# Performance work log

Measured on AMD Instinct MI355X. Metric: run time of the kernel, lower is better.

## Reference

```python
import jax, jax.numpy as jnp
import numpy as np

B, LV, LT, D, TD, H = 64, 1024, 128, 256, 1536, 4
HD = D // H
KEEP_RATIO = 0.5
K = min(max(int(np.ceil(LV * KEEP_RATIO)), 1), LV)
ND = LV - K  # number of dropped tokens
EPS_NORM = 1e-12


def setup_inputs() -> dict:
    key = jax.random.key(0)
    ks = jax.random.split(key, 9)
    s = 0.02
    return {
        "hidden_v": jax.random.normal(ks[0], (B, LV, D), jnp.float32),
        "hidden_t": jax.random.normal(ks[1], (B, LT, TD), jnp.float32),
        "senti_t": jax.random.normal(ks[2], (B, LT), jnp.float32),
        "mask_v": jnp.ones((B, LV), dtype=bool),
        "mask_t": jnp.ones((B, LT), dtype=bool),
        "W_t": jax.random.normal(ks[3], (D, TD), jnp.float32) * s,
        "b_t": jnp.zeros((D,), jnp.float32),
        "Wq": jax.random.normal(ks[4], (D, D), jnp.float32) * s,
        "bq": jnp.zeros((D,), jnp.float32),
        "Wk": jax.random.normal(ks[5], (D, D), jnp.float32) * s,
        "bk": jnp.zeros((D,), jnp.float32),
    }


def _l2norm(x):
    n = jnp.linalg.norm(x, axis=-1, keepdims=True)
    return x / jnp.maximum(n, EPS_NORM)


def _prune_one(V_b, score_b):
    """V_b: [LV, D], score_b: [LV] -> (V_merge [K, D], top_idx [K])."""
    _, top_idx = jax.lax.top_k(score_b, K)
    top_idx = jnp.sort(top_idx)
    V_keep = V_b[top_idx]                       # [K, D]
    drop_mask = jnp.ones((LV,), bool).at[top_idx].set(False)
    ar = jnp.arange(LV)
    drop_idx = jnp.sort(jnp.where(drop_mask, ar, LV + ar))[:ND]  # [ND], sorted
    V_drop = V_b[drop_idx]                      # [ND, D]
    score_drop = score_b[drop_idx]              # [ND]
    # bipartite cosine-similarity assignment of dropped -> kept
    sim = _l2norm(V_drop) @ _l2norm(V_keep).T   # [ND, K]
    assign = jnp.argmax(sim, axis=1)            # [ND]
    # per-cluster softmax over dropped-token scores (segment softmax)
    seg_max = jax.ops.segment_max(score_drop, assign, num_segments=K)
    w = jnp.exp(score_drop - seg_max[assign])
    denom = jax.ops.segment_sum(w, assign, num_segments=K)
    w = w / jnp.maximum(denom[assign], EPS_NORM)
    merged = jax.ops.segment_sum(w[:, None] * V_drop, assign, num_segments=K)
    has_member = jax.ops.segment_sum(jnp.ones((ND,), V_b.dtype), assign, num_segments=K) > 0
    V_merge = _l2norm(V_keep + merged)
    V_out = jnp.where(has_member[:, None], V_merge, V_keep)
    return V_out, top_idx


def reference(hidden_v, hidden_t, senti_t, mask_v, mask_t, W_t, b_t, Wq, bq, Wk, bk):
    mt = mask_t.astype(jnp.float32)
    # text projection + sentiment weights
    T = hidden_t @ W_t.T + b_t                                   # [B, LT, D]
    w_t = jnp.abs(senti_t) * mt
    w_t = w_t / (w_t.sum(axis=1, keepdims=True) + 1e-8)
    w_t = w_t * mt
    # cross-attention weights (averaged over heads); attn_out is unused by the module
    q = (hidden_v @ Wq.T + bq).reshape(B, LV, H, HD)
    k = (T @ Wk.T + bk).reshape(B, LT, H, HD)
    scores = jnp.einsum('bqhd,bkhd->bhqk', q, k) / np.sqrt(HD)   # [B, H, LV, LT]
    scores = jnp.where(mask_t[:, None, None, :], scores, -1e9)
    attn = jax.nn.softmax(scores, axis=-1).mean(axis=1)          # [B, LV, LT]
    score_v = jnp.einsum('bqk,bk->bq', attn, w_t)                # [B, LV]
    score_v = jnp.where(mask_v, score_v, -1e9)
    hidden_v_new, retained_indices = jax.vmap(_prune_one)(hidden_v, score_v)
    return hidden_v_new, retained_indices
```

## Files before the change

kernel.cpp:

```cpp
#include <hip/hip_runtime.h>
#include <math.h>

#define B_ 64
#define LV_ 1024
#define LT_ 128
#define D_ 256
#define TD_ 1536
#define H_ 4
#define HD_ 64
#define K_ 512
#define ND_ 512

__device__ float g_M[TD_ * D_];
__device__ float g_WqT[D_ * D_];
__device__ float g_WkT[D_ * D_];
__device__ float g_kbias[D_];
__device__ float g_wt[B_ * LT_];
__device__ float g_Kmat[(size_t)B_ * LT_ * D_];
__device__ float g_score[B_ * LV_];
__device__ int   g_tidx[B_ * K_];
__device__ int   g_didx[B_ * ND_];
__device__ float g_sdrop[B_ * ND_];
__device__ int   g_assign[B_ * ND_];
__device__ float g_kninv[B_ * K_];


__device__ __forceinline__ float f4c(const float4& v, int i) {
  return ((const float*)&v)[i];
}

__global__ __launch_bounds__(256) void prep1_kernel(
    const float* __restrict__ Wk, const float* __restrict__ Wq,
    const float* __restrict__ bt, const float* __restrict__ bk) {
  int bx = blockIdx.x, t = threadIdx.x;
  if (bx < D_) {
    g_WkT[bx * D_ + t] = Wk[t * D_ + bx];
  } else if (bx < 2 * D_) {
    int j = bx - D_;
    g_WqT[j * D_ + t] = Wq[t * D_ + j];
  } else {
    float acc = bk[t];
    for (int e = 0; e < D_; ++e) acc += bt[e] * Wk[t * D_ + e];
    g_kbias[t] = acc;
  }
}

__global__ __launch_bounds__(256) void prep2_kernel(const float* __restrict__ Wt) {
  int j0 = blockIdx.x * 16;
  int t = threadIdx.x;
  __shared__ float WtL[256 * 20];
  const float4* Wt4 = (const float4*)Wt;
#pragma unroll
  for (int i = 0; i < 4; ++i) {
    int idx = i * 256 + t;
    int e = idx >> 2, j4 = idx & 3;
    float4 v = Wt4[e * (TD_ / 4) + (j0 >> 2) + j4];
    WtL[e * 20 + 4 * j4 + 0] = v.x;
    WtL[e * 20 + 4 * j4 + 1] = v.y;
    WtL[e * 20 + 4 * j4 + 2] = v.z;
    WtL[e * 20 + 4 * j4 + 3] = v.w;
  }
  __syncthreads();
  float acc[16];
#pragma unroll
  for (int jj = 0; jj < 16; ++jj) acc[jj] = 0.f;
  for (int e = 0; e < D_; ++e) {
    float wk = g_WkT[e * D_ + t];
#pragma unroll
    for (int q4 = 0; q4 < 4; ++q4) {
      float4 w = *(const float4*)&WtL[e * 20 + 4 * q4];
      acc[4 * q4 + 0] += w.x * wk;
      acc[4 * q4 + 1] += w.y * wk;
      acc[4 * q4 + 2] += w.z * wk;
      acc[4 * q4 + 3] += w.w * wk;
    }
  }
#pragma unroll
  for (int jj = 0; jj < 16; ++jj) g_M[(j0 + jj) * D_ + t] = acc[jj];
}

__global__ __launch_bounds__(128) void wt_kernel(const float* __restrict__ senti) {
  int b = blockIdx.x, t = threadIdx.x;
  __shared__ float red[128];
  float v = fabsf(senti[b * LT_ + t]);
  red[t] = v;
  __syncthreads();
  for (int s = 64; s > 0; s >>= 1) {
    if (t < s) red[t] += red[t + s];
    __syncthreads();
  }
  g_wt[b * LT_ + t] = v / (red[0] + 1e-8f);
}

__global__ __launch_bounds__(256) void kproj_kernel(const float* __restrict__ ht) {
  int b = blockIdx.x >> 3;
  int l0 = (blockIdx.x & 7) * 16;
  int t = threadIdx.x;
  __shared__ float htT[256 * 20];
  int lq = t >> 6;
  int dq = t & 63;
  float acc[4][4];
#pragma unroll
  for (int li = 0; li < 4; ++li)
#pragma unroll
    for (int di = 0; di < 4; ++di) acc[li][di] = 0.f;
  const float4* M4 = (const float4*)g_M;
  const float4* ht4 = (const float4*)ht;
  for (int e0 = 0; e0 < TD_; e0 += 256) {
    __syncthreads();
#pragma unroll
    for (int i = 0; i < 4; ++i) {
      int idx = i * 256 + t;
      int e4 = idx >> 4, l = idx & 15;
      float4 v = ht4[(size_t)(b * LT_ + l0 + l) * (TD_ / 4) + (e0 >> 2) + e4];
      htT[(4 * e4 + 0) * 20 + l] = v.x;
      htT[(4 * e4 + 1) * 20 + l] = v.y;
      htT[(4 * e4 + 2) * 20 + l] = v.z;
      htT[(4 * e4 + 3) * 20 + l] = v.w;
    }
    __syncthreads();
    for (int e = 0; e < 256; ++e) {
      float4 m = M4[(size_t)(e0 + e) * 64 + dq];
      float4 hl = *(const float4*)&htT[e * 20 + 4 * lq];
#pragma unroll
      for (int li = 0; li < 4; ++li) {
        float hs = f4c(hl, li);
        acc[li][0] += hs * m.x;
        acc[li][1] += hs * m.y;
        acc[li][2] += hs * m.z;
        acc[li][3] += hs * m.w;
      }
    }
  }
  float4 kb = *(const float4*)(g_kbias + 4 * dq);
#pragma unroll
  for (int li = 0; li < 4; ++li) {
    float4 o = make_float4(acc[li][0] + kb.x, acc[li][1] + kb.y,
                           acc[li][2] + kb.z, acc[li][3] + kb.w);
    ((float4*)g_Kmat)[(size_t)(b * LT_ + l0 + 4 * lq + li) * 64 + dq] = o;
  }
}

__global__ __launch_bounds__(256, 3) void score_kernel(
    const float* __restrict__ hv, const float* __restrict__ bq) {
  int b = blockIdx.y;
  int q0 = blockIdx.x * 32;
  int t = threadIdx.x;
  __shared__ float qR[32 * 256];
  __shared__ float kT[32 * 128];
  int co = t & 31;
  int rq = t >> 5;
  {
    float acc[4][8];
#pragma unroll
    for (int c = 0; c < 8; ++c) {
      float bqv = bq[8 * co + c];
#pragma unroll
      for (int ri = 0; ri < 4; ++ri) acc[ri][c] = bqv;
    }
    const float4* hv4 = (const float4*)(hv + ((size_t)b * LV_ + q0) * D_);
    for (int j4 = 0; j4 < 64; ++j4) {
      float4 hq[4];
#pragma unroll
      for (int ri = 0; ri < 4; ++ri) hq[ri] = hv4[(4 * rq + ri) * 64 + j4];
#pragma unroll
      for (int jj = 0; jj < 4; ++jj) {
        const float4* w4 = (const float4*)(g_WqT + (4 * j4 + jj) * D_ + 8 * co);
        float4 wa = w4[0], wb = w4[1];
#pragma unroll
        for (int ri = 0; ri < 4; ++ri) {
          float hvv = f4c(hq[ri], jj);
          acc[ri][0] += hvv * wa.x;
          acc[ri][1] += hvv * wa.y;
          acc[ri][2] += hvv * wa.z;
          acc[ri][3] += hvv * wa.w;
          acc[ri][4] += hvv * wb.x;
          acc[ri][5] += hvv * wb.y;
          acc[ri][6] += hvv * wb.z;
          acc[ri][7] += hvv * wb.w;
        }
      }
    }
    float4* qR4w = (float4*)qR;
#pragma unroll
    for (int ri = 0; ri < 4; ++ri) {
      qR4w[(4 * rq + ri) * 64 + 2 * co + 0] =
          make_float4(acc[ri][0], acc[ri][1], acc[ri][2], acc[ri][3]);
      qR4w[(4 * rq + ri) * 64 + 2 * co + 1] =
          make_float4(acc[ri][4], acc[ri][5], acc[ri][6], acc[ri][7]);
    }
  }
  int qq = rq;
  int kq = co;
  float4 wtv = ((const float4*)(g_wt + b * LT_))[kq];
  float svacc[4] = {0.f, 0.f, 0.f, 0.f};
  const float4* km4 = ((const float4*)g_Kmat) + (size_t)b * LT_ * 64;
  const float4* qR4 = (const float4*)qR;
  const float4* kT4 = (const float4*)kT;
  for (int h = 0; h < H_; ++h) {
    float sacc[4][4];
#pragma unroll
    for (int ri = 0; ri < 4; ++ri)
#pragma unroll
      for (int ki = 0; ki < 4; ++ki) sacc[ri][ki] = 0.f;
    for (int half = 0; half < 2; ++half) {
      __syncthreads();
      {
#pragma unroll
        for (int i = 0; i < 4; ++i) {
          int idx = i * 256 + t;
          int k = idx >> 3, d4 = idx & 7;
          float4 v = km4[k * 64 + h * 16 + half * 8 + d4];
          int ksw = ((((k >> 2) ^ d4) << 2) | (k & 3));
          kT[(4 * d4 + 0) * 128 + ksw] = v.x;
          kT[(4 * d4 + 1) * 128 + ksw] = v.y;
          kT[(4 * d4 + 2) * 128 + ksw] = v.z;
          kT[(4 * d4 + 3) * 128 + ksw] = v.w;
        }
      }
      __syncthreads();
#pragma unroll
      for (int d4l = 0; d4l < 8; ++d4l) {
        float4 qv[4], kv[4];
#pragma unroll
        for (int ri = 0; ri < 4; ++ri)
          qv[ri] = qR4[(4 * qq + ri) * 64 + h * 16 + half * 8 + d4l];
#pragma unroll
        for (int dd = 0; dd < 4; ++dd)
          kv[dd] = kT4[(4 * d4l + dd) * 32 + (kq ^ d4l)];
#pragma unroll
        for (int dd = 0; dd < 4; ++dd)
#pragma unroll
          for (int ri = 0; ri < 4; ++ri) {
            float qs = f4c(qv[ri], dd);
            sacc[ri][0] += qs * kv[dd].x;
            sacc[ri][1] += qs * kv[dd].y;
            sacc[ri][2] += qs * kv[dd].z;
            sacc[ri][3] += qs * kv[dd].w;
          }
      }
    }
#pragma unroll
    for (int ri = 0; ri < 4; ++ri) {
      float s0 = sacc[ri][0] * 0.125f, s1 = sacc[ri][1] * 0.125f;
      float s2 = sacc[ri][2] * 0.125f, s3 = sacc[ri][3] * 0.125f;
      float m = fmaxf(fmaxf(s0, s1), fmaxf(s2, s3));
#pragma unroll
      for (int off = 16; off > 0; off >>= 1) m = fmaxf(m, __shfl_xor(m, off));
      float e0 = expf(s0 - m), e1 = expf(s1 - m);
      float e2 = expf(s2 - m), e3 = expf(s3 - m);
      float es = e0 + e1 + e2 + e3;
      float cs = e0 * wtv.x + e1 * wtv.y + e2 * wtv.z + e3 * wtv.w;
#pragma unroll
      for (int off = 16; off > 0; off >>= 1) {
        es += __shfl_xor(es, off);
        cs += __shfl_xor(cs, off);
      }
      svacc[ri] += cs / es;
    }
  }
  if (kq == 0) {
#pragma unroll
    for (int ri = 0; ri < 4; ++ri)
      g_score[(size_t)b * LV_ + q0 + 4 * qq + ri] = svacc[ri] * 0.25f;
  }
}

__global__ __launch_bounds__(1024) void topk_kernel(float* __restrict__ out_idx) {
  int b = blockIdx.x, t = threadIdx.x;
  __shared__ float s[LV_];
  __shared__ unsigned char keep[LV_];
  s[t] = g_score[(size_t)b * LV_ + t];
  __syncthreads();
  float mys = s[t];
  int cnt = 0;
  for (int jj = 0; jj < LV_; ++jj) {
    float sj = s[jj];
    cnt += (sj > mys || (sj == mys && jj < t)) ? 1 : 0;
  }
  int kp = (cnt < K_) ? 1 : 0;
  keep[t] = (unsigned char)kp;
  __syncthreads();
  int pos = 0;
  for (int jj = 0; jj < t; ++jj) pos += keep[jj];
  if (kp) {
    g_tidx[b * K_ + pos] = t;
    out_idx[b * K_ + pos] = (float)t;
  } else {
    int dp = t - pos;
    g_didx[b * ND_ + dp] = t;
    g_sdrop[b * ND_ + dp] = mys;
  }
}

__global__ __launch_bounds__(256) void knorm_kernel(const float* __restrict__ hv) {
  int b = blockIdx.y;
  int k = blockIdx.x * 256 + threadIdx.x;
  int src = g_tidx[b * K_ + k];
  const float4* row = (const float4*)(hv + ((size_t)b * LV_ + src) * D_);
  float acc = 0.f;
  for (int c = 0; c < 64; ++c) {
    float4 v = row[c];
    acc += v.x * v.x;
    acc += v.y * v.y;
    acc += v.z * v.z;
    acc += v.w * v.w;
  }
  g_kninv[b * K_ + k] = 1.f / fmaxf(sqrtf(acc), 1e-12f);
}

__global__ __launch_bounds__(128) void assign_kernel(const float* __restrict__ hv) {
  int b = blockIdx.y;
  int n0 = blockIdx.x * 32;
  int t = threadIdx.x;
  __shared__ float VdL[32][260];
  __shared__ float VkL[16][260];
  __shared__ float bestvL[32][8];
  __shared__ int bestkL[32][8];
  {
    int r0 = t >> 5, c0 = t & 31;
#pragma unroll
    for (int p = 0; p < 8; ++p) {
      int r = r0 + 4 * p;
      const float* src = hv + ((size_t)b * LV_ + g_didx[b * ND_ + n0 + r]) * D_;
      for (int c = c0; c < D_; c += 32) VdL[r][c] = src[c];
    }
  }
  int nq = t >> 3;
  int kq = t & 7;
  float bv0 = -INFINITY, bv1 = -INFINITY;
  int bk0 = 0, bk1 = 0;
  for (int kt = 0; kt < 32; ++kt) {
    __syncthreads();
    {
      int r0 = t >> 5, c0 = t & 31;
#pragma unroll
      for (int p = 0; p < 4; ++p) {
        int r = r0 + 4 * p;
        const float* src = hv + ((size_t)b * LV_ + g_tidx[b * K_ + kt * 16 + r]) * D_;
        for (int c = c0; c < D_; c += 32) VkL[r][c] = src[c];
      }
    }
    __syncthreads();
    const float4* vd0 = (const float4*)(&VdL[2 * nq][0]);
    const float4* vd1 = (const float4*)(&VdL[2 * nq + 1][0]);
    const float4* vk0 = (const float4*)(&VkL[2 * kq][0]);
    const float4* vk1 = (const float4*)(&VkL[2 * kq + 1][0]);
    float4 a00 = {0, 0, 0, 0}, a01 = {0, 0, 0, 0}, a10 = {0, 0, 0, 0}, a11 = {0, 0, 0, 0};
#pragma unroll 8
    for (int d4 = 0; d4 < 64; ++d4) {
      float4 x0 = vd0[d4], x1 = vd1[d4];
      float4 y0 = vk0[d4], y1 = vk1[d4];
      a00.x += x0.x * y0.x; a00.y += x0.y * y0.y; a00.z += x0.z * y0.z; a00.w += x0.w * y0.w;
      a01.x += x0.x * y1.x; a01.y += x0.y * y1.y; a01.z += x0.z * y1.z; a01.w += x0.w * y1.w;
      a10.x += x1.x * y0.x; a10.y += x1.y * y0.y; a10.z += x1.z * y0.z; a10.w += x1.w * y0.w;
      a11.x += x1.x * y1.x; a11.y += x1.y * y1.y; a11.z += x1.z * y1.z; a11.w += x1.w * y1.w;
    }
    float s00 = (a00.x + a00.y) + (a00.z + a00.w);
    float s01 = (a01.x + a01.y) + (a01.z + a01.w);
    float s10 = (a10.x + a10.y) + (a10.z + a10.w);
    float s11 = (a11.x + a11.y) + (a11.z + a11.w);
    int kg0 = kt * 16 + 2 * kq, kg1 = kg0 + 1;
    float kn0 = g_kninv[b * K_ + kg0], kn1 = g_kninv[b * K_ + kg1];
    float v00 = s00 * kn0, v01 = s01 * kn1, v10 = s10 * kn0, v11 = s11 * kn1;
    if (v00 > bv0) { bv0 = v00; bk0 = kg0; }
    if (v01 > bv0) { bv0 = v01; bk0 = kg1; }
    if (v10 > bv1) { bv1 = v10; bk1 = kg0; }
    if (v11 > bv1) { bv1 = v11; bk1 = kg1; }
  }
  bestvL[2 * nq][kq] = bv0; bestkL[2 * nq][kq] = bk0;
  bestvL[2 * nq + 1][kq] = bv1; bestkL[2 * nq + 1][kq] = bk1;
  __syncthreads();
  if (t < 32) {
    float bvf = bestvL[t][0];
    int bkf = bestkL[t][0];
    for (int q = 1; q < 8; ++q) {
      float v = bestvL[t][q];
      int kx = bestkL[t][q];
      if (v > bvf || (v == bvf && kx < bkf)) { bvf = v; bkf = kx; }
    }
    g_assign[b * ND_ + n0 + t] = bkf;
  }
}

__global__ __launch_bounds__(64) void merge_kernel(
    const float* __restrict__ hv, float* __restrict__ out_v) {
  int b = blockIdx.y, k = blockIdx.x;
  int lane = threadIdx.x;
  __shared__ int mem[ND_];
  int base = 0;
  for (int c = 0; c < ND_; c += 64) {
    int a = g_assign[b * ND_ + c + lane];
    unsigned long long msk = __ballot(a == k);
    if (a == k) {
      int pos = base + __popcll(msk & ((1ULL << lane) - 1ULL));
      mem[pos] = c + lane;
    }
    base += __popcll(msk);
  }
  __syncthreads();
  int src = g_tidx[b * K_ + k];
  float4 vk = ((const float4*)(hv + ((size_t)b * LV_ + src) * D_))[lane];
  float4 res;
  if (base > 0) {
    float mx = -INFINITY;
    for (int i = lane; i < base; i += 64) mx = fmaxf(mx, g_sdrop[b * ND_ + mem[i]]);
#pragma unroll
    for (int o = 32; o > 0; o >>= 1) mx = fmaxf(mx, __shfl_xor(mx, o));
    float dsum = 0.f;
    for (int i = lane; i < base; i += 64) dsum += expf(g_sdrop[b * ND_ + mem[i]] - mx);
#pragma unroll
    for (int o = 32; o > 0; o >>= 1) dsum += __shfl_xor(dsum, o);
    dsum = fmaxf(dsum, 1e-12f);
    float4 acc = {0.f, 0.f, 0.f, 0.f};
    for (int i = 0; i < base; ++i) {
      int n = mem[i];
      float w = expf(g_sdrop[b * ND_ + n] - mx) / dsum;
      float4 ud = ((const float4*)(hv + ((size_t)b * LV_ + g_didx[b * ND_ + n]) * D_))[lane];
      acc.x += w * ud.x; acc.y += w * ud.y;
      acc.z += w * ud.z; acc.w += w * ud.w;
    }
    float4 s4 = {vk.x + acc.x, vk.y + acc.y, vk.z + acc.z, vk.w + acc.w};
    float ss = s4.x * s4.x + s4.y * s4.y + s4.z * s4.z + s4.w * s4.w;
#pragma unroll
    for (int o = 32; o > 0; o >>= 1) ss += __shfl_xor(ss, o);
    float scale = 1.f / fmaxf(sqrtf(ss), 1e-12f);
    res.x = s4.x * scale; res.y = s4.y * scale; res.z = s4.z * scale; res.w = s4.w * scale;
  } else {
    res = vk;
  }
  ((float4*)(out_v + ((size_t)b * K_ + k) * D_))[lane] = res;
}

extern "C" void kernel_launch(void* const* d_in, const int* in_sizes, int n_in,
                              void* d_out, int out_size, void* d_ws, size_t ws_size,
                              hipStream_t stream) {
  const float* hv = (const float*)d_in[0];
  const float* ht = (const float*)d_in[1];
  const float* senti = (const float*)d_in[2];
  const float* Wt = (const float*)d_in[5];
  const float* bt = (const float*)d_in[6];
  const float* Wq = (const float*)d_in[7];
  const float* bq = (const float*)d_in[8];
  const float* Wk = (const float*)d_in[9];
  const float* bk = (const float*)d_in[10];
  (void)in_sizes; (void)n_in; (void)out_size; (void)d_ws; (void)ws_size;

  float* out_v = (float*)d_out;
  float* out_idx = out_v + (size_t)B_ * K_ * D_;

  hipLaunchKernelGGL(prep1_kernel, dim3(2 * D_ + 1), dim3(256), 0, stream, Wk, Wq, bt, bk);
  hipLaunchKernelGGL(prep2_kernel, dim3(TD_ / 16), dim3(256), 0, stream, Wt);
  hipLaunchKernelGGL(wt_kernel, dim3(B_), dim3(128), 0, stream, senti);
  hipLaunchKernelGGL(kproj_kernel, dim3(B_ * 8), dim3(256), 0, stream, ht);
  hipLaunchKernelGGL(score_kernel, dim3(LV_ / 32, B_), dim3(256), 0, stream, hv, bq);
  hipLaunchKernelGGL(topk_kernel, dim3(B_), dim3(1024), 0, stream, out_idx);
  hipLaunchKernelGGL(knorm_kernel, dim3(2, B_), dim3(256), 0, stream, hv);
  hipLaunchKernelGGL(assign_kernel, dim3(ND_ / 32, B_), dim3(128), 0, stream, hv);
  hipLaunchKernelGGL(merge_kernel, dim3(K_, B_), dim3(64), 0, stream, hv, out_v);
}
```

Before: 944.3 us.

## Retile assign kernel with 4x4 register blocking and swizzled transposed K tile

Rewrites the dropped-to-kept cosine-similarity argmax kernel to use 256 threads, each computing a 4x4 block of dot products over a 32x128 tile, staged in D chunks of 32 through shared memory. The kept-token tile is stored transposed with an XOR swizzle to avoid bank conflicts and allow float4 reads. The aim is to raise arithmetic intensity per shared-memory load and cut the old 16-row K tiling's many sync iterations. The trade-off is higher register pressure from 64 accumulators and more barriers per K tile. The final reduction now scans 32 partial results per row.

```diff
diff --git a/kernel.cpp b/kernel.cpp
--- a/kernel.cpp
+++ b/kernel.cpp
@@ -309,74 +309,107 @@
   g_kninv[b * K_ + k] = 1.f / fmaxf(sqrtf(acc), 1e-12f);
 }
 
-__global__ __launch_bounds__(128) void assign_kernel(const float* __restrict__ hv) {
+__global__ __launch_bounds__(256, 3) void assign_kernel(const float* __restrict__ hv) {
   int b = blockIdx.y;
   int n0 = blockIdx.x * 32;
   int t = threadIdx.x;
-  __shared__ float VdL[32][260];
-  __shared__ float VkL[16][260];
-  __shared__ float bestvL[32][8];
-  __shared__ int bestkL[32][8];
-  {
-    int r0 = t >> 5, c0 = t & 31;
-#pragma unroll
-    for (int p = 0; p < 8; ++p) {
-      int r = r0 + 4 * p;
-      const float* src = hv + ((size_t)b * LV_ + g_didx[b * ND_ + n0 + r]) * D_;
-      for (int c = c0; c < D_; c += 32) VdL[r][c] = src[c];
-    }
-  }
-  int nq = t >> 3;
-  int kq = t & 7;
-  float bv0 = -INFINITY, bv1 = -INFINITY;
-  int bk0 = 0, bk1 = 0;
-  for (int kt = 0; kt < 32; ++kt) {
-    __syncthreads();
-    {
-      int r0 = t >> 5, c0 = t & 31;
-#pragma unroll
-      for (int p = 0; p < 4; ++p) {
-        int r = r0 + 4 * p;
-        const float* src = hv + ((size_t)b * LV_ + g_tidx[b * K_ + kt * 16 + r]) * D_;
-        for (int c = c0; c < D_; c += 32) VkL[r][c] = src[c];
-      }
-    }
-    __syncthreads();
-    const float4* vd0 = (const float4*)(&VdL[2 * nq][0]);
-    const float4* vd1 = (const float4*)(&VdL[2 * nq + 1][0]);
-    const float4* vk0 = (const float4*)(&VkL[2 * kq][0]);
-    const float4* vk1 = (const float4*)(&VkL[2 * kq + 1][0]);
-    float4 a00 = {0, 0, 0, 0}, a01 = {0, 0, 0, 0}, a10 = {0, 0, 0, 0}, a11 = {0, 0, 0, 0};
-#pragma unroll 8
-    for (int d4 = 0; d4 < 64; ++d4) {
-      float4 x0 = vd0[d4], x1 = vd1[d4];
-      float4 y0 = vk0[d4], y1 = vk1[d4];
-      a00.x += x0.x * y0.x; a00.y += x0.y * y0.y; a00.z += x0.z * y0.z; a00.w += x0.w * y0.w;
-      a01.x += x0.x * y1.x; a01.y += x0.y * y1.y; a01.z += x0.z * y1.z; a01.w += x0.w * y1.w;
-      a10.x += x1.x * y0.x; a10.y += x1.y * y0.y; a10.z += x1.z * y0.z; a10.w += x1.w * y0.w;
-      a11.x += x1.x * y1.x; a11.y += x1.y * y1.y; a11.z += x1.z * y1.z; a11.w += x1.w * y1.w;
-    }
-    float s00 = (a00.x + a00.y) + (a00.z + a00.w);
-    float s01 = (a01.x + a01.y) + (a01.z + a01.w);
-    float s10 = (a10.x + a10.y) + (a10.z + a10.w);
-    float s11 = (a11.x + a11.y) + (a11.z + a11.w);
-    int kg0 = kt * 16 + 2 * kq, kg1 = kg0 + 1;
-    float kn0 = g_kninv[b * K_ + kg0], kn1 = g_kninv[b * K_ + kg1];
-    float v00 = s00 * kn0, v01 = s01 * kn1, v10 = s10 * kn0, v11 = s11 * kn1;
-    if (v00 > bv0) { bv0 = v00; bk0 = kg0; }
-    if (v01 > bv0) { bv0 = v01; bk0 = kg1; }
-    if (v10 > bv1) { bv1 = v10; bk1 = kg0; }
-    if (v11 > bv1) { bv1 = v11; bk1 = kg1; }
-  }
-  bestvL[2 * nq][kq] = bv0; bestkL[2 * nq][kq] = bk0;
-  bestvL[2 * nq + 1][kq] = bv1; bestkL[2 * nq + 1][kq] = bk1;
+  __shared__ float smem[32 * 9 * 4 + 32 * 128];
+  float* VdL = smem;
+  float* VkT = smem + 1152;
+  float* bestv = smem;
+  int* bestk = (int*)(smem + 1024);
+
+  int tn = t >> 5;
+  int tk = t & 31;
+  int rstage = t >> 3;
+  int c8 = t & 7;
+
+  int didx_t = g_didx[b * ND_ + n0 + rstage];
+  const float4* vd_src = (const float4*)(hv + ((size_t)b * LV_ + didx_t) * D_);
+
+  float bv[4] = {-INFINITY, -INFINITY, -INFINITY, -INFINITY};
+  int bk[4] = {0, 0, 0, 0};
+
+  for (int kt = 0; kt < 4; ++kt) {
+    const float4* vk_src[4];
+#pragma unroll
+    for (int i = 0; i < 4; ++i) {
+      int kl = i * 32 + rstage;
+      int tix = g_tidx[b * K_ + kt * 128 + kl];
+      vk_src[i] = (const float4*)(hv + ((size_t)b * LV_ + tix) * D_);
+    }
+    float4 kn4 = ((const float4*)(g_kninv + (size_t)b * K_ + kt * 128))[tk];
+    float acc[4][4][4];
+#pragma unroll
+    for (int ri = 0; ri < 4; ++ri)
+#pragma unroll
+      for (int kj = 0; kj < 4; ++kj)
+#pragma unroll
+        for (int c = 0; c < 4; ++c) acc[ri][kj][c] = 0.f;
+    for (int dc = 0; dc < 8; ++dc) {
+      __syncthreads();
+      {
+        float4 v = vd_src[dc * 8 + c8];
+        ((float4*)VdL)[rstage * 9 + c8] = v;
+      }
+#pragma unroll
+      for (int i = 0; i < 4; ++i) {
+        int kl = i * 32 + rstage;
+        float4 v = vk_src[i][dc * 8 + c8];
+        int col = ((((kl >> 2) ^ c8) << 2) | (kl & 3));
+        VkT[(4 * c8 + 0) * 128 + col] = v.x;
+        VkT[(4 * c8 + 1) * 128 + col] = v.y;
+        VkT[(4 * c8 + 2) * 128 + col] = v.z;
+        VkT[(4 * c8 + 3) * 128 + col] = v.w;
+      }
+      __syncthreads();
+      const float4* VdL4 = (const float4*)VdL;
+      const float4* VkT4 = (const float4*)VkT;
+#pragma unroll
+      for (int d4l = 0; d4l < 8; ++d4l) {
+        float4 vd[4], kv[4];
+#pragma unroll
+        for (int ri = 0; ri < 4; ++ri)
+          vd[ri] = VdL4[(4 * tn + ri) * 9 + d4l];
+#pragma unroll
+        for (int dd = 0; dd < 4; ++dd)
+          kv[dd] = VkT4[(4 * d4l + dd) * 32 + (tk ^ d4l)];
+#pragma unroll
+        for (int dd = 0; dd < 4; ++dd)
+#pragma unroll
+          for (int ri = 0; ri < 4; ++ri) {
+            float a = f4c(vd[ri], dd);
+            acc[ri][0][dd] += a * kv[dd].x;
+            acc[ri][1][dd] += a * kv[dd].y;
+            acc[ri][2][dd] += a * kv[dd].z;
+            acc[ri][3][dd] += a * kv[dd].w;
+          }
+      }
+    }
+#pragma unroll
+    for (int ri = 0; ri < 4; ++ri) {
+#pragma unroll
+      for (int kj = 0; kj < 4; ++kj) {
+        float s = (acc[ri][kj][0] + acc[ri][kj][1]) + (acc[ri][kj][2] + acc[ri][kj][3]);
+        float v = s * f4c(kn4, kj);
+        int kg = kt * 128 + 4 * tk + kj;
+        if (v > bv[ri]) { bv[ri] = v; bk[ri] = kg; }
+      }
+    }
+  }
+  __syncthreads();
+#pragma unroll
+  for (int ri = 0; ri < 4; ++ri) {
+    bestv[(4 * tn + ri) * 32 + tk] = bv[ri];
+    bestk[(4 * tn + ri) * 32 + tk] = bk[ri];
+  }
   __syncthreads();
   if (t < 32) {
-    float bvf = bestvL[t][0];
-    int bkf = bestkL[t][0];
-    for (int q = 1; q < 8; ++q) {
-      float v = bestvL[t][q];
-      int kx = bestkL[t][q];
+    float bvf = bestv[t * 32];
+    int bkf = bestk[t * 32];
+    for (int q = 1; q < 32; ++q) {
+      float v = bestv[t * 32 + q];
+      int kx = bestk[t * 32 + q];
       if (v > bvf || (v == bvf && kx < bkf)) { bvf = v; bkf = kx; }
     }
     g_assign[b * ND_ + n0 + t] = bkf;
@@ -456,6 +489,6 @@
   hipLaunchKernelGGL(score_kernel, dim3(LV_ / 32, B_), dim3(256), 0, stream, hv, bq);
   hipLaunchKernelGGL(topk_kernel, dim3(B_), dim3(1024), 0, stream, out_idx);
   hipLaunchKernelGGL(knorm_kernel, dim3(2, B_), dim3(256), 0, stream, hv);
-  hipLaunchKernelGGL(assign_kernel, dim3(ND_ / 32, B_), dim3(128), 0, stream, hv);
+  hipLaunchKernelGGL(assign_kernel, dim3(ND_ / 32, B_), dim3(128 / 4 * 8), 0, stream, hv);
   hipLaunchKernelGGL(merge_kernel, dim3(K_, B_), dim3(64), 0, stream, hv, out_v);
 }
```

New measurement: 796.3 us. -15.7%, faster.
